# Optimization experiments

Hardware: AMD Instinct MI355X
Metric: run time of the kernel (lower is better)

Reference implementation:

```python
import jax, jax.numpy as jnp
import numpy as np

NUM_HIGH = 3
CHANNELS = 3

def _gauss_kernel(channels):
    k = jnp.array([[1., 4., 6., 4., 1.],
                   [4., 16., 24., 16., 4.],
                   [6., 24., 36., 24., 6.],
                   [4., 16., 24., 16., 4.],
                   [1., 4., 6., 4., 1.]], dtype=jnp.float32) / 256.0
    # depthwise kernel layout OIHW with I=1, O=channels
    return jnp.broadcast_to(k, (channels, 1, 5, 5))

def conv_gauss(img, kernel):
    # reflect-pad by 2 on H,W then depthwise (grouped) 5x5 conv, VALID
    p = jnp.pad(img, ((0, 0), (0, 0), (2, 2), (2, 2)), mode='reflect')
    return jax.lax.conv_general_dilated(
        p, kernel, window_strides=(1, 1), padding='VALID',
        feature_group_count=img.shape[1],
        dimension_numbers=('NCHW', 'OIHW', 'NCHW'))

def downsample(x):
    return x[:, :, ::2, ::2]

def upsample(x, kernel):
    B, C, H, W = x.shape
    x_up = jnp.zeros((B, C, 2 * H, 2 * W), dtype=x.dtype).at[:, :, ::2, ::2].set(x)
    return conv_gauss(x_up, 4.0 * kernel)

def setup_inputs() -> dict:
    key = jax.random.key(0)
    img = jax.random.normal(key, (8, CHANNELS, 1024, 1024), dtype=jnp.float32)
    kernel = _gauss_kernel(CHANNELS)
    return {"img": img, "kernel": kernel}

def reference(img, kernel):
    # pyramid_decom: Laplacian pyramid (H,W divisible by 2**NUM_HIGH, so no interpolate)
    current = img
    pyr = []
    for _ in range(NUM_HIGH):
        filtered = conv_gauss(current, kernel)
        down = downsample(filtered)
        up = upsample(down, kernel)
        pyr.append(current - up)
        current = down
    pyr.append(current)
    return tuple(pyr)
```

## Files before the change

### kernel.cpp

```cpp
#include <hip/hip_runtime.h>

#define TILE 64
#define SCP 76
#define TMP 77
#define SDP 35

__device__ __forceinline__ int refl(int t, int n) {
    if (t < 0) t = -t;
    if (t >= n) t = 2 * (n - 1) - t;
    return t;
}

__global__ __launch_bounds__(512, 8) void lap_level_kernel(
    const float* __restrict__ cur, float* __restrict__ lap,
    float* __restrict__ down, int H, int W)
{
    __shared__ float s_cur[72][SCP];
    __shared__ float s_tmp[34][TMP];
    __shared__ float s_down[34][SDP];

    const int x0 = blockIdx.x * TILE, y0 = blockIdx.y * TILE;
    const int img = blockIdx.z;
    const int Hh = H >> 1, Wh = W >> 1;
    const int tid = threadIdx.x;

    const float* curb = cur + (size_t)img * H * W;

    const bool border = (x0 == 0) | (y0 == 0) | (x0 + TILE == W) | (y0 + TILE == H);
    if (!border) {
        const float* src = curb + (size_t)(y0 - 4) * W + (x0 - 4);
        for (int k = tid; k < 72 * 18; k += 512) {
            unsigned r = (unsigned)k / 18u;
            unsigned c4 = ((unsigned)k - r * 18u) * 4u;
            *(float4*)&s_cur[r][c4] = *(const float4*)(src + (size_t)r * W + c4);
        }
    } else {
        for (int k = tid; k < 72 * 72; k += 512) {
            unsigned r = (unsigned)k / 72u;
            unsigned c = (unsigned)k - r * 72u;
            s_cur[r][c] = curb[(size_t)refl(y0 - 4 + (int)r, H) * W
                               + refl(x0 - 4 + (int)c, W)];
        }
    }
    __syncthreads();

    for (int k = tid; k < 34 * 18; k += 512) {
        unsigned a = (unsigned)k / 18u;
        unsigned c4 = ((unsigned)k - a * 18u) * 4u;
        float4 r0 = *(const float4*)&s_cur[2 * a + 0][c4];
        float4 r1 = *(const float4*)&s_cur[2 * a + 1][c4];
        float4 r2 = *(const float4*)&s_cur[2 * a + 2][c4];
        float4 r3 = *(const float4*)&s_cur[2 * a + 3][c4];
        float4 r4 = *(const float4*)&s_cur[2 * a + 4][c4];
        s_tmp[a][c4 + 0] = r0.x + 4.f * r1.x + 6.f * r2.x + 4.f * r3.x + r4.x;
        s_tmp[a][c4 + 1] = r0.y + 4.f * r1.y + 6.f * r2.y + 4.f * r3.y + r4.y;
        s_tmp[a][c4 + 2] = r0.z + 4.f * r1.z + 6.f * r2.z + 4.f * r3.z + r4.z;
        s_tmp[a][c4 + 3] = r0.w + 4.f * r1.w + 6.f * r2.w + 4.f * r3.w + r4.w;
    }
    __syncthreads();

    float* downb = down + (size_t)img * Hh * Wh;
    for (int k = tid; k < 34 * 34; k += 512) {
        unsigned a = (unsigned)k / 34u;
        unsigned b = (unsigned)k - a * 34u;
        const float* t = &s_tmp[a][2 * b];
        float v = (t[0] + 4.f * t[1] + 6.f * t[2] + 4.f * t[3] + t[4]) * (1.f / 256.f);
        s_down[a][b] = v;
        if (a - 1u < 32u && b - 1u < 32u)
            downb[(size_t)((y0 >> 1) + (int)a - 1) * Wh + ((x0 >> 1) + (int)b - 1)] = v;
    }
    __syncthreads();

    const int tx = tid & 15, ty = tid >> 4;
    float d0[4], d1[4], d2[4];
#pragma unroll
    for (int c = 0; c < 4; ++c) {
        d0[c] = s_down[ty + 0][2 * tx + c];
        d1[c] = s_down[ty + 1][2 * tx + c];
        d2[c] = s_down[ty + 2][2 * tx + c];
    }
    float ce[4], co[4];
#pragma unroll
    for (int c = 0; c < 4; ++c) {
        ce[c] = d0[c] + 6.f * d1[c] + d2[c];
        co[c] = 4.f * (d1[c] + d2[c]);
    }
    float4 cve = *(const float4*)&s_cur[4 + 2 * ty][4 + 4 * tx];
    float4 cvo = *(const float4*)&s_cur[5 + 2 * ty][4 + 4 * tx];
    float4 oe, oo;
    oe.x = cve.x - (ce[0] + 6.f * ce[1] + ce[2]) * (1.f / 64.f);
    oe.y = cve.y - 4.f * (ce[1] + ce[2]) * (1.f / 64.f);
    oe.z = cve.z - (ce[1] + 6.f * ce[2] + ce[3]) * (1.f / 64.f);
    oe.w = cve.w - 4.f * (ce[2] + ce[3]) * (1.f / 64.f);
    oo.x = cvo.x - (co[0] + 6.f * co[1] + co[2]) * (1.f / 64.f);
    oo.y = cvo.y - 4.f * (co[1] + co[2]) * (1.f / 64.f);
    oo.z = cvo.z - (co[1] + 6.f * co[2] + co[3]) * (1.f / 64.f);
    oo.w = cvo.w - 4.f * (co[2] + co[3]) * (1.f / 64.f);

    float* lapb = lap + (size_t)img * H * W;
    const int i0 = y0 + 2 * ty, j0 = x0 + 4 * tx;
    *(float4*)(lapb + (size_t)i0 * W + j0) = oe;
    *(float4*)(lapb + (size_t)(i0 + 1) * W + j0) = oo;
}

extern "C" void kernel_launch(void* const* d_in, const int* in_sizes, int n_in,
                              void* d_out, int out_size, void* d_ws, size_t ws_size,
                              hipStream_t stream) {
    const float* img = (const float*)d_in[0];
    float* out = (float*)d_out;

    const long long BC = 8LL * 3;
    const long long n0 = BC * 1024 * 1024;
    const long long n1 = BC * 512 * 512;
    const long long n2 = BC * 256 * 256;

    float* out0 = out;
    float* out1 = out0 + n0;
    float* out2 = out1 + n1;
    float* out3 = out2 + n2;

    float* ws0 = (float*)d_ws;
    float* ws1 = ws0 + n1;

    lap_level_kernel<<<dim3(1024 / TILE, 1024 / TILE, (int)BC), 512, 0, stream>>>(
        img, out0, ws0, 1024, 1024);
    lap_level_kernel<<<dim3(512 / TILE, 512 / TILE, (int)BC), 512, 0, stream>>>(
        ws0, out1, ws1, 512, 512);
    lap_level_kernel<<<dim3(256 / TILE, 256 / TILE, (int)BC), 512, 0, stream>>>(
        ws1, out2, out3, 256, 256);
}
```

Baseline: 84.48 us.

## Fuse vertical blur into global loads and shrink tile to 64x32

```diff
diff --git a/kernel.cpp b/kernel.cpp
--- a/kernel.cpp
+++ b/kernel.cpp
@@ -1,8 +1,10 @@
 #include <hip/hip_runtime.h>
 
-#define TILE 64
-#define SCP 76
-#define TMP 77
+#define TW 64
+#define TH 32
+#define DR 18
+#define DC 34
+#define TMPP 76
 #define SDP 35
 
 __device__ __forceinline__ int refl(int t, int n) {
@@ -11,63 +13,69 @@
     return t;
 }
 
-__global__ __launch_bounds__(512, 8) void lap_level_kernel(
+__global__ __launch_bounds__(256, 8) void lap_level_kernel(
     const float* __restrict__ cur, float* __restrict__ lap,
     float* __restrict__ down, int H, int W)
 {
-    __shared__ float s_cur[72][SCP];
-    __shared__ float s_tmp[34][TMP];
-    __shared__ float s_down[34][SDP];
+    __shared__ float s_tmp[DR][TMPP];
+    __shared__ float s_down[DR][SDP];
 
-    const int x0 = blockIdx.x * TILE, y0 = blockIdx.y * TILE;
+    const int x0 = blockIdx.x * TW, y0 = blockIdx.y * TH;
     const int img = blockIdx.z;
     const int Hh = H >> 1, Wh = W >> 1;
     const int tid = threadIdx.x;
 
     const float* curb = cur + (size_t)img * H * W;
 
-    const bool border = (x0 == 0) | (y0 == 0) | (x0 + TILE == W) | (y0 + TILE == H);
+    const bool border = (x0 == 0) | (y0 == 0) | (x0 + TW == W) | (y0 + TH == H);
     if (!border) {
-        const float* src = curb + (size_t)(y0 - 4) * W + (x0 - 4);
-        for (int k = tid; k < 72 * 18; k += 512) {
-            unsigned r = (unsigned)k / 18u;
-            unsigned c4 = ((unsigned)k - r * 18u) * 4u;
-            *(float4*)&s_cur[r][c4] = *(const float4*)(src + (size_t)r * W + c4);
+        for (int k = tid; k < DR * 18; k += 256) {
+            unsigned a = (unsigned)k / 18u;
+            unsigned c4 = ((unsigned)k - a * 18u) * 4u;
+            const float* p = curb + (size_t)(y0 + 2 * (int)a - 4) * W + (x0 - 4 + (int)c4);
+            float4 r0 = *(const float4*)(p);
+            float4 r1 = *(const float4*)(p + (size_t)W);
+            float4 r2 = *(const float4*)(p + (size_t)2 * W);
+            float4 r3 = *(const float4*)(p + (size_t)3 * W);
+            float4 r4 = *(const float4*)(p + (size_t)4 * W);
+            float4 t;
+            t.x = r0.x + 4.f * r1.x + 6.f * r2.x + 4.f * r3.x + r4.x;
+            t.y = r0.y + 4.f * r1.y + 6.f * r2.y + 4.f * r3.y + r4.y;
+            t.z = r0.z + 4.f * r1.z + 6.f * r2.z + 4.f * r3.z + r4.z;
+            t.w = r0.w + 4.f * r1.w + 6.f * r2.w + 4.f * r3.w + r4.w;
+            *(float4*)&s_tmp[a][c4] = t;
         }
     } else {
-        for (int k = tid; k < 72 * 72; k += 512) {
-            unsigned r = (unsigned)k / 72u;
-            unsigned c = (unsigned)k - r * 72u;
-            s_cur[r][c] = curb[(size_t)refl(y0 - 4 + (int)r, H) * W
-                               + refl(x0 - 4 + (int)c, W)];
+        for (int k = tid; k < DR * 72; k += 256) {
+            unsigned a = (unsigned)k / 72u;
+            unsigned c = (unsigned)k - a * 72u;
+            int gx = refl(x0 - 4 + (int)c, W);
+            int r0 = y0 + 2 * (int)a - 4;
+            float acc = 0.f;
+            const float wv[5] = {1.f, 4.f, 6.f, 4.f, 1.f};
+#pragma unroll
+            for (int u = 0; u < 5; ++u)
+                acc += wv[u] * curb[(size_t)refl(r0 + u, H) * W + gx];
+            s_tmp[a][c] = acc;
         }
     }
     __syncthreads();
 
-    for (int k = tid; k < 34 * 18; k += 512) {
-        unsigned a = (unsigned)k / 18u;
-        unsigned c4 = ((unsigned)k - a * 18u) * 4u;
-        float4 r0 = *(const float4*)&s_cur[2 * a + 0][c4];
-        float4 r1 = *(const float4*)&s_cur[2 * a + 1][c4];
-        float4 r2 = *(const float4*)&s_cur[2 * a + 2][c4];
-        float4 r3 = *(const float4*)&s_cur[2 * a + 3][c4];
-        float4 r4 = *(const float4*)&s_cur[2 * a + 4][c4];
-        s_tmp[a][c4 + 0] = r0.x + 4.f * r1.x + 6.f * r2.x + 4.f * r3.x + r4.x;
-        s_tmp[a][c4 + 1] = r0.y + 4.f * r1.y + 6.f * r2.y + 4.f * r3.y + r4.y;
-        s_tmp[a][c4 + 2] = r0.z + 4.f * r1.z + 6.f * r2.z + 4.f * r3.z + r4.z;
-        s_tmp[a][c4 + 3] = r0.w + 4.f * r1.w + 6.f * r2.w + 4.f * r3.w + r4.w;
-    }
-    __syncthreads();
-
     float* downb = down + (size_t)img * Hh * Wh;
-    for (int k = tid; k < 34 * 34; k += 512) {
-        unsigned a = (unsigned)k / 34u;
-        unsigned b = (unsigned)k - a * 34u;
-        const float* t = &s_tmp[a][2 * b];
-        float v = (t[0] + 4.f * t[1] + 6.f * t[2] + 4.f * t[3] + t[4]) * (1.f / 256.f);
-        s_down[a][b] = v;
-        if (a - 1u < 32u && b - 1u < 32u)
-            downb[(size_t)((y0 >> 1) + (int)a - 1) * Wh + ((x0 >> 1) + (int)b - 1)] = v;
+    for (int k = tid; k < DR * 17; k += 256) {
+        unsigned a = (unsigned)k / 17u;
+        unsigned b2 = (unsigned)k - a * 17u;
+        float4 A = *(const float4*)&s_tmp[a][4 * b2];
+        float4 B = *(const float4*)&s_tmp[a][4 * b2 + 4];
+        float v0 = (A.x + 4.f * A.y + 6.f * A.z + 4.f * A.w + B.x) * (1.f / 256.f);
+        float v1 = (A.z + 4.f * A.w + 6.f * B.x + 4.f * B.y + B.z) * (1.f / 256.f);
+        s_down[a][2 * b2] = v0;
+        s_down[a][2 * b2 + 1] = v1;
+        if (a - 1u < 16u) {
+            size_t rowoff = (size_t)((y0 >> 1) - 1 + (int)a) * Wh + ((x0 >> 1) - 1);
+            if (b2 >= 1u) downb[rowoff + 2 * b2] = v0;
+            if (b2 <= 15u) downb[rowoff + 2 * b2 + 1] = v1;
+        }
     }
     __syncthreads();
 
@@ -85,8 +93,10 @@
         ce[c] = d0[c] + 6.f * d1[c] + d2[c];
         co[c] = 4.f * (d1[c] + d2[c]);
     }
-    float4 cve = *(const float4*)&s_cur[4 + 2 * ty][4 + 4 * tx];
-    float4 cvo = *(const float4*)&s_cur[5 + 2 * ty][4 + 4 * tx];
+    const int i0 = y0 + 2 * ty, j0 = x0 + 4 * tx;
+    const float* cvp = curb + (size_t)i0 * W + j0;
+    float4 cve = *(const float4*)(cvp);
+    float4 cvo = *(const float4*)(cvp + (size_t)W);
     float4 oe, oo;
     oe.x = cve.x - (ce[0] + 6.f * ce[1] + ce[2]) * (1.f / 64.f);
     oe.y = cve.y - 4.f * (ce[1] + ce[2]) * (1.f / 64.f);
@@ -98,7 +108,6 @@
     oo.w = cvo.w - 4.f * (co[2] + co[3]) * (1.f / 64.f);
 
     float* lapb = lap + (size_t)img * H * W;
-    const int i0 = y0 + 2 * ty, j0 = x0 + 4 * tx;
     *(float4*)(lapb + (size_t)i0 * W + j0) = oe;
     *(float4*)(lapb + (size_t)(i0 + 1) * W + j0) = oo;
 }
@@ -122,10 +131,10 @@
     float* ws0 = (float*)d_ws;
     float* ws1 = ws0 + n1;
 
-    lap_level_kernel<<<dim3(1024 / TILE, 1024 / TILE, (int)BC), 512, 0, stream>>>(
+    lap_level_kernel<<<dim3(1024 / TW, 1024 / TH, (int)BC), 256, 0, stream>>>(
         img, out0, ws0, 1024, 1024);
-    lap_level_kernel<<<dim3(512 / TILE, 512 / TILE, (int)BC), 512, 0, stream>>>(
+    lap_level_kernel<<<dim3(512 / TW, 512 / TH, (int)BC), 256, 0, stream>>>(
         ws0, out1, ws1, 512, 512);
-    lap_level_kernel<<<dim3(256 / TILE, 256 / TILE, (int)BC), 512, 0, stream>>>(
+    lap_level_kernel<<<dim3(256 / TW, 256 / TH, (int)BC), 256, 0, stream>>>(
         ws1, out2, out3, 256, 256);
 }
```

New measurement: 81.03 us. 1.04x faster.
